# Optimization experiments

Measured on AMD Instinct MI355X. Metric: run time of the kernel, lower is better.

## Reference

```python
import jax, jax.numpy as jnp
import numpy as np

N = 1024
H = 4096
W = 4096
K_COUNTS = 10
IOU_T = 0.5
NEG = -1e30  # -inf stand-in for unrecorded groups


def _box_iou(b):
    # b: [N,4] xyxy pixel coords -> [N,N] IoU (torchvision.ops.box_iou)
    area = (b[:, 2] - b[:, 0]) * (b[:, 3] - b[:, 1])
    ix1 = jnp.maximum(b[:, None, 0], b[None, :, 0])
    iy1 = jnp.maximum(b[:, None, 1], b[None, :, 1])
    ix2 = jnp.minimum(b[:, None, 2], b[None, :, 2])
    iy2 = jnp.minimum(b[:, None, 3], b[None, :, 3])
    inter = jnp.clip(ix2 - ix1, 0.0) * jnp.clip(iy2 - iy1, 0.0)
    return inter / (area[:, None] + area[None, :] - inter)


def _c_wsl(iou_gt, scores, counts):
    # Faithful vectorized c_wsl_fast: for every start box i, greedily sweep
    # j = i+1..N-1 adding boxes compatible (IoU <= T) with all current members;
    # when a group hits `counts` at the TOP of a j-iteration it is recorded
    # (check-before-add semantics, so a group completed at j = N-1 is never
    # recorded, matching the original break-based control flow). The final
    # answer is the LAST start achieving the max recorded score (>= update).
    n = scores.shape[0]
    starts = jnp.arange(n)
    carry0 = (
        jnp.eye(n, dtype=bool),            # sel[i, k]: box k in group of start i
        jnp.ones(n, jnp.int32),            # group sizes
        scores,                            # group scores
        jnp.zeros(n, bool),                # recorded flag (== break)
        jnp.full(n, NEG, scores.dtype),    # recorded score
        jnp.zeros((n, n), bool),           # recorded membership
    )

    def step(c, xs):
        j, sj, iou_j = xs  # iou_j = iou_gt[j] (> T bool row; matrix symmetric)
        sel, size, score, rec, rec_score, rec_sel = c
        active = (j > starts) & (~rec)
        do_rec = active & (size == counts)
        rec_sel = jnp.where(do_rec[:, None], sel, rec_sel)
        rec_score = jnp.where(do_rec, score, rec_score)
        rec = rec | do_rec
        compat = ~jnp.any(sel & iou_j[None, :], axis=1)
        add = active & (~do_rec) & (size < counts) & compat
        sel = sel.at[:, j].set(sel[:, j] | add)
        size = size + add.astype(size.dtype)
        score = score + jnp.where(add, sj, jnp.zeros((), score.dtype))
        return (sel, size, score, rec, rec_score, rec_sel), None

    (_, _, _, rec, rec_score, rec_sel), _ = jax.lax.scan(
        step, carry0, (starts, scores, iou_gt))
    masked = jnp.where(rec, rec_score, NEG)
    best = (n - 1) - jnp.argmax(masked[::-1])  # last argmax == '>=' update rule
    return jnp.where(jnp.any(rec), rec_sel[best], jnp.zeros(n, bool))


def reference(bbox, obj_scores, probs, counts):
    Hh, Ww = probs.shape
    # score_bbox_heatmap(reduction='mean'): mean of probs[y1:y2, x1:x2] per box,
    # computed exactly for all boxes with a zero-padded summed-area table.
    sat = jnp.pad(jnp.cumsum(jnp.cumsum(probs, axis=0), axis=1), ((1, 0), (1, 0)))
    x1 = jnp.clip(jnp.floor(bbox[:, 0]).astype(jnp.int32), 0, Ww)
    y1 = jnp.clip(jnp.floor(bbox[:, 1]).astype(jnp.int32), 0, Hh)
    x2 = jnp.clip(jnp.floor(bbox[:, 2]).astype(jnp.int32), 0, Ww)
    y2 = jnp.clip(jnp.floor(bbox[:, 3]).astype(jnp.int32), 0, Hh)
    sums = sat[y2, x2] - sat[y1, x2] - sat[y2, x1] + sat[y1, x1]
    cnt = jnp.maximum((y2 - y1) * (x2 - x1), 1).astype(probs.dtype)
    box_scores = sums / cnt
    # agg_score_method == 'mean'
    scores = 0.5 * (obj_scores + box_scores)
    # sort descending, then greedy IoU grouping on sorted boxes
    order = jnp.argsort(-scores)
    bbox_s = bbox[order]
    scores_s = scores[order]
    iou_gt = _box_iou(bbox_s) > IOU_T
    sel = _c_wsl(iou_gt, scores_s, counts)
    return scores_s * sel.astype(scores_s.dtype)


def setup_inputs() -> dict:
    key = jax.random.key(0)
    k1, k2, k3, k4, k5, k6 = jax.random.split(key, 6)
    cx = jax.random.uniform(k1, (N,), minval=0.15, maxval=0.85) * W
    cy = jax.random.uniform(k2, (N,), minval=0.15, maxval=0.85) * H
    bw = jnp.maximum(jax.random.uniform(k3, (N,), minval=0.02, maxval=0.25) * W, 8.0)
    bh = jnp.maximum(jax.random.uniform(k4, (N,), minval=0.02, maxval=0.25) * H, 8.0)
    bbox = jnp.stack([cx - bw / 2, cy - bh / 2, cx + bw / 2, cy + bh / 2], axis=1)
    obj_scores = jax.random.uniform(k5, (N,))
    probs = jax.random.uniform(k6, (H, W))
    return {"bbox": bbox, "obj_scores": obj_scores, "probs": probs, "counts": K_COUNTS}
```

## Files before the change

kernel.cpp:

```cpp
#include <hip/hip_runtime.h>

#define HH 4096
#define WW 4096
#define NB 1024
#define NCHUNK 64
#define CROWS 64
#define IOU_T 0.5f

typedef unsigned long long u64;

constexpr size_t OFF_COORDS = 0;
constexpr size_t OFF_RD     = OFF_COORDS + (size_t)NB * 16;
constexpr size_t OFF_PART   = OFF_RD     + (size_t)HH * 16;
constexpr size_t OFF_SC64   = OFF_PART   + (size_t)NCHUNK * WW * 8;
constexpr size_t OFF_ORDER  = OFF_SC64   + (size_t)NB * 8;
constexpr size_t OFF_IOU    = OFF_ORDER  + (size_t)NB * 4;
constexpr size_t OFF_RECSC  = OFF_IOU    + (size_t)NB * 16 * 8;
constexpr size_t OFF_RECSEL = OFF_RECSC  + (size_t)NB * 8;
constexpr size_t OFF_CC     = OFF_RECSEL + (size_t)NB * 16 * 8;


__global__ void __launch_bounds__(1024) k_setup(const float* __restrict__ bbox,
                        int4* coords, int4* rowdesc) {
    __shared__ int lf[HH];
    __shared__ int xlo[HH];
    __shared__ int xhi[HH];
    __shared__ int psum[256];
    int t = threadIdx.x;
    for (int k = t; k < HH; k += 1024) { lf[k] = 0; xlo[k] = WW; xhi[k] = 0; }
    __syncthreads();
    {
        int i = t;
        if (i < NB) {
            float b0 = bbox[i * 4 + 0], b1 = bbox[i * 4 + 1];
            float b2 = bbox[i * 4 + 2], b3 = bbox[i * 4 + 3];
            int x1 = min(max((int)floorf(b0), 0), WW);
            int y1 = min(max((int)floorf(b1), 0), HH);
            int x2 = min(max((int)floorf(b2), 0), WW);
            int y2 = min(max((int)floorf(b3), 0), HH);
            coords[i] = make_int4(x1, y1, x2, y2);
            if (y1 >= 1) {
                lf[y1 - 1] = 1;
                atomicMin(&xlo[y1 - 1], x1);
                atomicMax(&xhi[y1 - 1], x2);
            }
            if (y2 >= 1) {
                lf[y2 - 1] = 1;
                atomicMin(&xlo[y2 - 1], x1);
                atomicMax(&xhi[y2 - 1], x2);
            }
        }
    }
    __syncthreads();
    if (t < 256) {
        int base = t * 16;
        int s = 0;
        for (int k = 0; k < 16; k++) s += lf[base + k];
        psum[t] = s;
    }
    __syncthreads();
    if (t == 0) {
        int acc = 0;
        for (int k = 0; k < 256; k++) { int v = psum[k]; psum[k] = acc; acc += v; }
    }
    __syncthreads();
    if (t < 256) {
        int base = t * 16;
        int run = psum[t];
        for (int k = 0; k < 16; k++) {
            int r = base + k;
            int fl = lf[r];
            rowdesc[r] = make_int4(fl ? run : -1, xlo[r] >> 2, (xhi[r] + 3) >> 2, 0);
            run += fl;
        }
    }
}

__global__ void __launch_bounds__(256) k_stage(const float* __restrict__ probs,
        const int4* __restrict__ rowdesc,
        double* __restrict__ part, float* __restrict__ Cc) {
    int tid = blockIdx.x * 256 + threadIdx.x;
    int c  = tid >> 10;
    int xq = tid & 1023;
    const float4* p = (const float4*)probs + (size_t)c * CROWS * (WW / 4) + xq;
    const int4* rd = rowdesc + c * CROWS;
    float4* Cc4 = (float4*)Cc;
    double a0 = 0.0, a1 = 0.0, a2 = 0.0, a3 = 0.0;
    for (int r = 0; r < CROWS; r += 8) {
        float4 q[8];
        #pragma unroll
        for (int k = 0; k < 8; k++) q[k] = p[(size_t)(r + k) * (WW / 4)];
        #pragma unroll
        for (int k = 0; k < 8; k++) {
            a0 += (double)q[k].x; a1 += (double)q[k].y;
            a2 += (double)q[k].z; a3 += (double)q[k].w;
            int4 d = rd[r + k];
            if (d.x >= 0 && xq >= d.y && xq < d.z)
                Cc4[(size_t)d.x * (WW / 4) + xq] =
                    make_float4((float)a0, (float)a1, (float)a2, (float)a3);
        }
    }
    double2* pp = (double2*)(part + (size_t)c * WW) + xq * 2;
    pp[0] = make_double2(a0, a1);
    pp[1] = make_double2(a2, a3);
}

__global__ void k_chunkscan(double* __restrict__ part) {
    int x = blockIdx.x * blockDim.x + threadIdx.x;
    double carry = 0.0;
    for (int g = 0; g < NCHUNK / 16; g++) {
        double v[16];
        #pragma unroll
        for (int k = 0; k < 16; k++) v[k] = part[(size_t)(g * 16 + k) * WW + x];
        #pragma unroll
        for (int k = 0; k < 16; k++) { double tv = v[k]; v[k] = carry; carry += tv; }
        #pragma unroll
        for (int k = 0; k < 16; k++) part[(size_t)(g * 16 + k) * WW + x] = v[k];
    }
}

__global__ void __launch_bounds__(64) k_boxsum(const int4* __restrict__ coords,
                         const float* __restrict__ obj,
                         const int4* __restrict__ rowdesc, const float* __restrict__ Cc,
                         const double* __restrict__ part,
                         double* sc64) {
    int i = blockIdx.x;
    int lane = threadIdx.x;
    int4 cd = coords[i];
    bool h1 = (cd.y >= 1), h2 = (cd.w >= 1);
    int s1 = h1 ? rowdesc[cd.y - 1].x : 0;
    int s2 = h2 ? rowdesc[cd.w - 1].x : 0;
    const float*  r2 = Cc   + (size_t)(h2 ? s2 : 0) * WW;
    const double* q2 = part + (size_t)(h2 ? ((cd.w - 1) >> 6) : 0) * WW;
    const float*  r1 = Cc   + (size_t)(h1 ? s1 : 0) * WW;
    const double* q1 = part + (size_t)(h1 ? ((cd.y - 1) >> 6) : 0) * WW;
    double s = 0.0;
    for (int x = cd.x + lane; x < cd.z; x += 64) {
        double v2 = h2 ? ((double)r2[x] + q2[x]) : 0.0;
        double v1 = h1 ? ((double)r1[x] + q1[x]) : 0.0;
        s += (v2 - v1);
    }
    #pragma unroll
    for (int off = 32; off > 0; off >>= 1) s += __shfl_down(s, off);
    if (lane == 0) {
        long long cnt = (long long)(cd.w - cd.y) * (long long)(cd.z - cd.x);
        if (cnt < 1) cnt = 1;
        double box = s / (double)cnt;
        sc64[i] = 0.5 * ((double)obj[i] + box);
    }
}

__global__ void __launch_bounds__(128) k_rank(const double* __restrict__ sc64,
                                              int* __restrict__ order) {
    __shared__ double s[NB];
    int t = threadIdx.x;
    for (int k = t; k < NB; k += 128) s[k] = sc64[k];
    __syncthreads();
    int i = blockIdx.x * 128 + t;
    double si = s[i];
    int rank = 0;
    #pragma unroll 8
    for (int j = 0; j < NB; j++) {
        double sj = s[j];
        rank += (sj > si) || (sj == si && j < i);
    }
    order[rank] = i;
}

__global__ void k_iou(const int* __restrict__ order, const float* __restrict__ bbox,
                      u64* __restrict__ ioub) {
    int tid = blockIdx.x * blockDim.x + threadIdx.x;
    int i = tid >> 10;
    int j = tid & (NB - 1);
    float4 a = ((const float4*)bbox)[order[i]];
    float4 b = ((const float4*)bbox)[order[j]];
    float ai = (a.z - a.x) * (a.w - a.y);
    float aj = (b.z - b.x) * (b.w - b.y);
    float ix1 = fmaxf(a.x, b.x), iy1 = fmaxf(a.y, b.y);
    float ix2 = fminf(a.z, b.z), iy2 = fminf(a.w, b.w);
    float iw = fmaxf(ix2 - ix1, 0.0f), ih = fmaxf(iy2 - iy1, 0.0f);
    float inter = iw * ih;
    float iou_v = inter / (ai + aj - inter);
    bool bit = iou_v > IOU_T;
    u64 m = __ballot(bit);
    if ((threadIdx.x & 63) == 0) ioub[(size_t)i * 16 + (j >> 6)] = m;
}

__global__ void __launch_bounds__(64) k_group(const u64* __restrict__ ioub,
                        const int* __restrict__ order,
                        const double* __restrict__ sc64,
                        const int* __restrict__ counts,
                        double* __restrict__ recsc,
                        u64* __restrict__ recsel) {
    __shared__ double ssd_s[NB];
    int t = threadIdx.x;
    int i = blockIdx.x * 64 + t;
    for (int k = t; k < NB; k += 64) ssd_s[k] = sc64[order[k]];
    __syncthreads();
    int K = counts[0];
    u64 inc[16], sel[16];
    int wi = i >> 6, bi = i & 63;
    #pragma unroll
    for (int w = 0; w < 16; w++) {
        inc[w] = ioub[(size_t)i * 16 + w];
        sel[w] = (w == wi) ? (1ULL << bi) : 0ULL;
    }
    int size = 1;
    double score = ssd_s[i];
    int last = i;
    #pragma unroll
    for (int w = 0; w < 16; w++) {
        if (w < wi || size >= K) continue;
        u64 avail = ~inc[w];
        if (w == wi) avail &= (bi == 63) ? 0ULL : (~0ULL << (bi + 1));
        while (avail != 0ULL && size < K) {
            int b = __builtin_ctzll(avail);
            int j = (w << 6) + b;
            sel[w] |= 1ULL << b;
            size++;
            score += ssd_s[j];
            last = j;
            const u64* rj = ioub + (size_t)j * 16;
            #pragma unroll
            for (int w2 = 0; w2 < 16; w2++) inc[w2] |= rj[w2];
            avail &= ~inc[w];
            avail &= ~(1ULL << b);
        }
    }
    int rec = (size == K) && (last < NB - 1);
    recsc[i] = rec ? score : -1e300;
    #pragma unroll
    for (int w = 0; w < 16; w++) recsel[(size_t)i * 16 + w] = sel[w];
}

__global__ void __launch_bounds__(1024) k_final(const double* __restrict__ recsc,
                        const u64* __restrict__ recsel,
                        const int* __restrict__ order,
                        const double* __restrict__ sc64, float* __restrict__ out) {
    __shared__ double bsc[NB];
    __shared__ int bidx[NB];
    __shared__ int best_s, any_s;
    int t = threadIdx.x;
    bsc[t] = recsc[t];
    bidx[t] = t;
    __syncthreads();
    for (int st = 512; st > 0; st >>= 1) {
        if (t < st) {
            double a = bsc[t], b2 = bsc[t + st];
            if (b2 > a || (b2 == a && bidx[t + st] > bidx[t])) {
                bsc[t] = b2;
                bidx[t] = bidx[t + st];
            }
        }
        __syncthreads();
    }
    if (t == 0) { best_s = bidx[0]; any_s = (bsc[0] > -1e299) ? 1 : 0; }
    __syncthreads();
    float v = 0.0f;
    if (any_s && ((recsel[(size_t)best_s * 16 + (t >> 6)] >> (t & 63)) & 1ULL))
        v = (float)sc64[order[t]];
    out[t] = v;
}


extern "C" void kernel_launch(void* const* d_in, const int* in_sizes, int n_in,
                              void* d_out, int out_size, void* d_ws, size_t ws_size,
                              hipStream_t stream) {
    const float* bbox  = (const float*)d_in[0];
    const float* obj   = (const float*)d_in[1];
    const float* probs = (const float*)d_in[2];
    const int*   counts = (const int*)d_in[3];
    float* out = (float*)d_out;

    char* w = (char*)d_ws;
    int4*   coords  = (int4*)(w + OFF_COORDS);
    int4*   rowdesc = (int4*)(w + OFF_RD);
    double* part    = (double*)(w + OFF_PART);
    double* sc64    = (double*)(w + OFF_SC64);
    int*    order   = (int*)(w + OFF_ORDER);
    u64*    ioub    = (u64*)(w + OFF_IOU);
    double* recsc   = (double*)(w + OFF_RECSC);
    u64*    recsel  = (u64*)(w + OFF_RECSEL);
    float*  Cc      = (float*)(w + OFF_CC);

    k_setup<<<1, 1024, 0, stream>>>(bbox, coords, rowdesc);
    k_stage<<<(NCHUNK * WW / 4) / 256, 256, 0, stream>>>(probs, rowdesc, part, Cc);
    k_chunkscan<<<WW / 256, 256, 0, stream>>>(part);
    k_boxsum<<<NB, 64, 0, stream>>>(coords, obj, rowdesc, Cc, part, sc64);
    k_rank<<<NB / 128, 128, 0, stream>>>(sc64, order);
    k_iou<<<(NB * NB) / 256, 256, 0, stream>>>(order, bbox, ioub);
    k_group<<<NB / 64, 64, 0, stream>>>(ioub, order, sc64, counts, recsc, recsel);
    k_final<<<1, 1024, 0, stream>>>(recsc, recsel, order, sc64, out);
}
```

Measured before the change: 182.3 us.

## Fuse final argmax into group kernel via last-block counter; parallelize setup scan

Removes the separate k_final launch by having the last k_group block, detected through an atomic counter reset in k_setup, perform the best-group reduction and write the output. The serial 256-element prefix scan in k_setup becomes a wavefront shuffle scan, and k_stage caches the row descriptors in shared memory. This saves one kernel launch and some serial work, at the cost of thread fences, an atomic, and a single-wave final reduction.

New measurement: 179.7 us. No clear change (-1.4%).

```diff
diff --git a/kernel.cpp b/kernel.cpp
--- a/kernel.cpp
+++ b/kernel.cpp
@@ -14,41 +14,41 @@
 constexpr size_t OFF_PART   = OFF_RD     + (size_t)HH * 16;
 constexpr size_t OFF_SC64   = OFF_PART   + (size_t)NCHUNK * WW * 8;
 constexpr size_t OFF_ORDER  = OFF_SC64   + (size_t)NB * 8;
-constexpr size_t OFF_IOU    = OFF_ORDER  + (size_t)NB * 4;
+constexpr size_t OFF_CTR    = OFF_ORDER  + (size_t)NB * 4;
+constexpr size_t OFF_IOU    = OFF_CTR    + 64;
 constexpr size_t OFF_RECSC  = OFF_IOU    + (size_t)NB * 16 * 8;
 constexpr size_t OFF_RECSEL = OFF_RECSC  + (size_t)NB * 8;
 constexpr size_t OFF_CC     = OFF_RECSEL + (size_t)NB * 16 * 8;
 
 
 __global__ void __launch_bounds__(1024) k_setup(const float* __restrict__ bbox,
-                        int4* coords, int4* rowdesc) {
+                        int4* coords, int4* rowdesc, int* ctr) {
     __shared__ int lf[HH];
     __shared__ int xlo[HH];
     __shared__ int xhi[HH];
     __shared__ int psum[256];
     int t = threadIdx.x;
+    if (t == 0) *ctr = 0;
     for (int k = t; k < HH; k += 1024) { lf[k] = 0; xlo[k] = WW; xhi[k] = 0; }
     __syncthreads();
-    {
+    if (t < NB) {
         int i = t;
-        if (i < NB) {
-            float b0 = bbox[i * 4 + 0], b1 = bbox[i * 4 + 1];
-            float b2 = bbox[i * 4 + 2], b3 = bbox[i * 4 + 3];
-            int x1 = min(max((int)floorf(b0), 0), WW);
-            int y1 = min(max((int)floorf(b1), 0), HH);
-            int x2 = min(max((int)floorf(b2), 0), WW);
-            int y2 = min(max((int)floorf(b3), 0), HH);
-            coords[i] = make_int4(x1, y1, x2, y2);
-            if (y1 >= 1) {
-                lf[y1 - 1] = 1;
-                atomicMin(&xlo[y1 - 1], x1);
-                atomicMax(&xhi[y1 - 1], x2);
-            }
-            if (y2 >= 1) {
-                lf[y2 - 1] = 1;
-                atomicMin(&xlo[y2 - 1], x1);
-                atomicMax(&xhi[y2 - 1], x2);
-            }
+        float b0 = bbox[i * 4 + 0], b1 = bbox[i * 4 + 1];
+        float b2 = bbox[i * 4 + 2], b3 = bbox[i * 4 + 3];
+        int x1 = min(max((int)floorf(b0), 0), WW);
+        int y1 = min(max((int)floorf(b1), 0), HH);
+        int x2 = min(max((int)floorf(b2), 0), WW);
+        int y2 = min(max((int)floorf(b3), 0), HH);
+        coords[i] = make_int4(x1, y1, x2, y2);
+        if (y1 >= 1) {
+            lf[y1 - 1] = 1;
+            atomicMin(&xlo[y1 - 1], x1);
+            atomicMax(&xhi[y1 - 1], x2);
+        }
+        if (y2 >= 1) {
+            lf[y2 - 1] = 1;
+            atomicMin(&xlo[y2 - 1], x1);
+            atomicMax(&xhi[y2 - 1], x2);
         }
     }
     __syncthreads();
@@ -59,9 +59,21 @@
         psum[t] = s;
     }
     __syncthreads();
-    if (t == 0) {
-        int acc = 0;
-        for (int k = 0; k < 256; k++) { int v = psum[k]; psum[k] = acc; acc += v; }
+    if (t < 64) {
+        int v0 = psum[t * 4], v1 = psum[t * 4 + 1];
+        int v2 = psum[t * 4 + 2], v3 = psum[t * 4 + 3];
+        int lsum = v0 + v1 + v2 + v3;
+        int incs = lsum;
+        #pragma unroll
+        for (int off = 1; off < 64; off <<= 1) {
+            int n = __shfl_up(incs, off);
+            if (t >= off) incs += n;
+        }
+        int ex = incs - lsum;
+        psum[t * 4]     = ex;
+        psum[t * 4 + 1] = ex + v0;
+        psum[t * 4 + 2] = ex + v0 + v1;
+        psum[t * 4 + 3] = ex + v0 + v1 + v2;
     }
     __syncthreads();
     if (t < 256) {
@@ -79,11 +91,13 @@
 __global__ void __launch_bounds__(256) k_stage(const float* __restrict__ probs,
         const int4* __restrict__ rowdesc,
         double* __restrict__ part, float* __restrict__ Cc) {
+    __shared__ int4 rd_s[CROWS];
     int tid = blockIdx.x * 256 + threadIdx.x;
     int c  = tid >> 10;
     int xq = tid & 1023;
+    if (threadIdx.x < CROWS) rd_s[threadIdx.x] = rowdesc[c * CROWS + threadIdx.x];
+    __syncthreads();
     const float4* p = (const float4*)probs + (size_t)c * CROWS * (WW / 4) + xq;
-    const int4* rd = rowdesc + c * CROWS;
     float4* Cc4 = (float4*)Cc;
     double a0 = 0.0, a1 = 0.0, a2 = 0.0, a3 = 0.0;
     for (int r = 0; r < CROWS; r += 8) {
@@ -94,7 +108,7 @@
         for (int k = 0; k < 8; k++) {
             a0 += (double)q[k].x; a1 += (double)q[k].y;
             a2 += (double)q[k].z; a3 += (double)q[k].w;
-            int4 d = rd[r + k];
+            int4 d = rd_s[r + k];
             if (d.x >= 0 && xq >= d.y && xq < d.z)
                 Cc4[(size_t)d.x * (WW / 4) + xq] =
                     make_float4((float)a0, (float)a1, (float)a2, (float)a3);
@@ -191,8 +205,11 @@
                         const double* __restrict__ sc64,
                         const int* __restrict__ counts,
                         double* __restrict__ recsc,
-                        u64* __restrict__ recsel) {
+                        u64* __restrict__ recsel,
+                        int* __restrict__ ctr,
+                        float* __restrict__ out) {
     __shared__ double ssd_s[NB];
+    __shared__ int lastflag;
     int t = threadIdx.x;
     int i = blockIdx.x * 64 + t;
     for (int k = t; k < NB; k += 64) ssd_s[k] = sc64[order[k]];
@@ -231,35 +248,32 @@
     recsc[i] = rec ? score : -1e300;
     #pragma unroll
     for (int w = 0; w < 16; w++) recsel[(size_t)i * 16 + w] = sel[w];
-}
-
-__global__ void __launch_bounds__(1024) k_final(const double* __restrict__ recsc,
-                        const u64* __restrict__ recsel,
-                        const int* __restrict__ order,
-                        const double* __restrict__ sc64, float* __restrict__ out) {
-    __shared__ double bsc[NB];
-    __shared__ int bidx[NB];
-    __shared__ int best_s, any_s;
-    int t = threadIdx.x;
-    bsc[t] = recsc[t];
-    bidx[t] = t;
-    __syncthreads();
-    for (int st = 512; st > 0; st >>= 1) {
-        if (t < st) {
-            double a = bsc[t], b2 = bsc[t + st];
-            if (b2 > a || (b2 == a && bidx[t + st] > bidx[t])) {
-                bsc[t] = b2;
-                bidx[t] = bidx[t + st];
-            }
-        }
-        __syncthreads();
-    }
-    if (t == 0) { best_s = bidx[0]; any_s = (bsc[0] > -1e299) ? 1 : 0; }
-    __syncthreads();
-    float v = 0.0f;
-    if (any_s && ((recsel[(size_t)best_s * 16 + (t >> 6)] >> (t & 63)) & 1ULL))
-        v = (float)sc64[order[t]];
-    out[t] = v;
+    __threadfence();
+    if (t == 0) lastflag = (atomicAdd(ctr, 1) == (int)gridDim.x - 1);
+    __syncthreads();
+    if (!lastflag) return;
+    __threadfence();
+    double bs = -1e301; int bidx = 0;
+    for (int m = 0; m < 16; m++) {
+        int k = t * 16 + m;
+        double v = recsc[k];
+        if (v >= bs) { bs = v; bidx = k; }
+    }
+    #pragma unroll
+    for (int off = 32; off > 0; off >>= 1) {
+        double ob = __shfl_down(bs, off);
+        int oi = __shfl_down(bidx, off);
+        if (ob > bs || (ob == bs && oi > bidx)) { bs = ob; bidx = oi; }
+    }
+    bs = __shfl(bs, 0);
+    bidx = __shfl(bidx, 0);
+    int any = bs > -1e299;
+    for (int k = t; k < NB; k += 64) {
+        float v = 0.0f;
+        if (any && ((recsel[(size_t)bidx * 16 + (k >> 6)] >> (k & 63)) & 1ULL))
+            v = (float)ssd_s[k];
+        out[k] = v;
+    }
 }
 
 
@@ -278,17 +292,18 @@
     double* part    = (double*)(w + OFF_PART);
     double* sc64    = (double*)(w + OFF_SC64);
     int*    order   = (int*)(w + OFF_ORDER);
+    int*    ctr     = (int*)(w + OFF_CTR);
     u64*    ioub    = (u64*)(w + OFF_IOU);
     double* recsc   = (double*)(w + OFF_RECSC);
     u64*    recsel  = (u64*)(w + OFF_RECSEL);
     float*  Cc      = (float*)(w + OFF_CC);
 
-    k_setup<<<1, 1024, 0, stream>>>(bbox, coords, rowdesc);
+    k_setup<<<1, 1024, 0, stream>>>(bbox, coords, rowdesc, ctr);
     k_stage<<<(NCHUNK * WW / 4) / 256, 256, 0, stream>>>(probs, rowdesc, part, Cc);
     k_chunkscan<<<WW / 256, 256, 0, stream>>>(part);
     k_boxsum<<<NB, 64, 0, stream>>>(coords, obj, rowdesc, Cc, part, sc64);
     k_rank<<<NB / 128, 128, 0, stream>>>(sc64, order);
     k_iou<<<(NB * NB) / 256, 256, 0, stream>>>(order, bbox, ioub);
-    k_group<<<NB / 64, 64, 0, stream>>>(ioub, order, sc64, counts, recsc, recsel);
-    k_final<<<1, 1024, 0, stream>>>(recsc, recsel, order, sc64, out);
-}
+    k_group<<<NB / 64, 64, 0, stream>>>(ioub, order, sc64, counts, recsc, recsel,
+                                        ctr, out);
+}
```
